# Kernel tuning notes

Hardware: AMD Instinct MI355X
Metric: run time of the kernel (lower is better)

Reference implementation:

```python
import jax, jax.numpy as jnp
import numpy as np

B = 2000           # number of events (segments)
N = 1_000_000      # total points (sum of num_points)
D_IN, H, D_OUT = 16, 256, 128
EPS = 1e-5


def _layer_norm(x, g, b):
    m = x.mean(-1, keepdims=True)
    v = x.var(-1, keepdims=True)
    return (x - m) * jax.lax.rsqrt(v + EPS) * g + b


def setup_inputs() -> dict:
    key = jax.random.key(0)
    ks = jax.random.split(key, 8)
    # ragged counts, all positive, summing exactly to N
    rng = np.random.default_rng(0)
    counts = np.full(B, N // B, dtype=np.int64)
    d = rng.integers(-400, 401, size=B // 2)
    counts[: B // 2] += d
    counts[B // 2 :] -= d
    assert counts.sum() == N and (counts > 0).all()
    z_t = jax.random.normal(ks[0], (N, D_IN), dtype=jnp.float32)
    def lin(k, fi, fo):
        return jax.random.normal(k, (fi, fo), dtype=jnp.float32) / np.sqrt(fi)
    return {
        "z_t": z_t,
        "W1": lin(ks[1], D_IN, H), "b1": jnp.zeros((H,), jnp.float32),
        "g1": jnp.ones((H,), jnp.float32), "be1": jnp.zeros((H,), jnp.float32),
        "W2": lin(ks[2], H, H), "b2": jnp.zeros((H,), jnp.float32),
        "g2": jnp.ones((H,), jnp.float32), "be2": jnp.zeros((H,), jnp.float32),
        "W3": lin(ks[3], H, D_OUT), "b3": jnp.zeros((D_OUT,), jnp.float32),
        "num_points": jnp.asarray(counts, dtype=jnp.int64),
    }


def reference(z_t, W1, b1, g1, be1, W2, b2, g2, be2, W3, b3, num_points):
    # per-point phi MLP: Linear -> LN -> ReLU (x2) -> Linear
    h = jax.nn.relu(_layer_norm(z_t @ W1 + b1, g1, be1))
    h = jax.nn.relu(_layer_norm(h @ W2 + b2, g2, be2))
    phi = h @ W3 + b3                                  # [N, D_OUT]
    # fused ragged mean-pool + broadcast back (replaces split/stack/repeat_interleave)
    seg = jnp.repeat(jnp.arange(B), num_points, total_repeat_length=N)  # [N]
    sums = jax.ops.segment_sum(phi, seg, num_segments=B)                # [B, D_OUT]
    emb = sums / num_points[:, None].astype(phi.dtype)                  # mean pooling
    return emb[seg]                                                     # [N, D_OUT]
```

## Files before the change

kernel.cpp:

```cpp
#include <hip/hip_runtime.h>
#include <hip/hip_bf16.h>
#include <cstdint>
#include <cstddef>

#define NPTS  1000000
#define BSEG  2000
#define DIN   16
#define HDIM  256
#define DOUT  128
#define NTILE (NPTS / 32)
#define NWG   512

typedef __bf16          bf16x8 __attribute__((ext_vector_type(8)));
typedef unsigned short  us16x8 __attribute__((ext_vector_type(8)));
typedef unsigned int    u32x4  __attribute__((ext_vector_type(4)));
typedef float           f32x4  __attribute__((ext_vector_type(4)));

static __device__ __forceinline__ unsigned short f2bf(float x) {
    unsigned int u = __float_as_uint(x);
    u += 0x7fffu + ((u >> 16) & 1u);
    return (unsigned short)(u >> 16);
}

static __device__ __forceinline__ bf16x8 ldb8(const unsigned short* p) {
    u32x4 v = *(const u32x4*)p;
    return __builtin_bit_cast(bf16x8, v);
}
static __device__ __forceinline__ f32x4 mfma16(bf16x8 a, bf16x8 b, f32x4 c) {
    return __builtin_amdgcn_mfma_f32_16x16x32_bf16(a, b, c, 0, 0, 0);
}
static __device__ __forceinline__ void keep(bf16x8& v) {
    u32x4 u = __builtin_bit_cast(u32x4, v);
    unsigned a0 = u[0], a1 = u[1], a2 = u[2], a3 = u[3];
    asm volatile("" : "+v"(a0), "+v"(a1), "+v"(a2), "+v"(a3));
    u32x4 r; r[0] = a0; r[1] = a1; r[2] = a2; r[3] = a3;
    v = __builtin_bit_cast(bf16x8, r);
}

static __device__ __forceinline__ float rsum16(float x) {
    x += __builtin_bit_cast(float, __builtin_amdgcn_update_dpp(
             0, __builtin_bit_cast(int, x), 0x128, 0xf, 0xf, false));
    x += __builtin_bit_cast(float, __builtin_amdgcn_update_dpp(
             0, __builtin_bit_cast(int, x), 0x124, 0xf, 0xf, false));
    x += __builtin_bit_cast(float, __builtin_amdgcn_update_dpp(
             0, __builtin_bit_cast(int, x), 0x122, 0xf, 0xf, false));
    x += __builtin_bit_cast(float, __builtin_amdgcn_update_dpp(
             0, __builtin_bit_cast(int, x), 0x121, 0xf, 0xf, false));
    return x;
}

__global__ __launch_bounds__(1024) void scan_counts(const int* __restrict__ counts,
                                                    int* __restrict__ offsets) {
    __shared__ int a[2048];
    const int t = threadIdx.x;
    a[t]        = (t        < BSEG) ? counts[t]        : 0;
    a[t + 1024] = (t + 1024 < BSEG) ? counts[t + 1024] : 0;
    for (int s = 1; s < 2048; s <<= 1) {
        __syncthreads();
        int x1 = (t >= s) ? a[t - s] : 0;
        int x2 = a[t + 1024 - s];
        __syncthreads();
        a[t] += x1;
        a[t + 1024] += x2;
    }
    __syncthreads();
    if (t == 0) offsets[0] = 0;
    offsets[t + 1] = a[t];
    if (t + 1024 < BSEG) offsets[t + 1025] = a[t + 1024];
}

__global__ __launch_bounds__(256) void fill_seg(const int* __restrict__ offsets,
                                                unsigned short* __restrict__ seg) {
    const int b  = blockIdx.x;
    const int lo = offsets[b], hi = offsets[b + 1];
    for (int i = lo + threadIdx.x; i < hi; i += 256) seg[i] = (unsigned short)b;
}

__global__ __launch_bounds__(256) void prep_weights(const float* __restrict__ W1,
                                                    const float* __restrict__ W2,
                                                    unsigned short* __restrict__ w1t,
                                                    unsigned short* __restrict__ w2t) {
    const int i = blockIdx.x * 256 + threadIdx.x;
    if (i < HDIM * 32) {
        int n = i >> 5, k = i & 31;
        w1t[i] = (k < DIN) ? f2bf(W1[k * HDIM + n]) : (unsigned short)0;
    } else {
        int j = i - HDIM * 32;
        if (j < HDIM * HDIM) {
            int n = j >> 8, k = j & 255;
            w2t[j] = f2bf(W2[k * HDIM + n]);
        }
    }
}

__global__ __launch_bounds__(256, 2) void fused_phi_pool(
    const float* __restrict__ z,
    const unsigned short* __restrict__ w1t,
    const unsigned short* __restrict__ w2t,
    const float* __restrict__ b1, const float* __restrict__ g1, const float* __restrict__ be1,
    const float* __restrict__ b2, const float* __restrict__ g2, const float* __restrict__ be2,
    const unsigned short* __restrict__ seg,
    float* __restrict__ sums_h) {
    __shared__ __align__(16) unsigned short h1[32][264];
    __shared__ __align__(16) float part[2][32][8];
    __shared__ __align__(16) int seg_sm[2][32];

    const int tid  = threadIdx.x;
    const int wave = tid >> 6;
    const int lane = tid & 63;
    const int l15  = lane & 15;
    const int quad = lane >> 4;
    const int colw = wave * 64 + l15;
    const bool zlane = (quad < 2);

    bf16x8 bw1[4];
    bf16x8 bw2[4][8];
#pragma unroll
    for (int t = 0; t < 4; ++t) {
        const int n = (wave * 4 + t) * 16 + l15;
        bw1[t] = ldb8(w1t + n * 32 + quad * 8);
        keep(bw1[t]);
#pragma unroll
        for (int ks = 0; ks < 8; ++ks) {
            bw2[t][ks] = ldb8(w2t + n * 256 + ks * 32 + quad * 8);
            keep(bw2[t][ks]);
        }
    }
    float b1v[4], g1v[4], e1v[4], b2v[4], g2v[4], e2v[4];
#pragma unroll
    for (int t = 0; t < 4; ++t) {
        const int c = colw + t * 16;
        b1v[t] = b1[c]; g1v[t] = g1[c]; e1v[t] = be1[c];
        b2v[t] = b2[c]; g2v[t] = g2[c]; e2v[t] = be2[c];
    }

    float4 zn[2][2];
    {
        const int base0 = blockIdx.x * 32;
        if (zlane) {
#pragma unroll
            for (int mb = 0; mb < 2; ++mb) {
                const float* zp = z + (size_t)(base0 + mb * 16 + l15) * DIN + quad * 8;
                zn[mb][0] = *(const float4*)zp;
                zn[mb][1] = *(const float4*)(zp + 4);
            }
        }
    }

    int p = 0;
    for (int tile = blockIdx.x; tile < NTILE; tile += NWG, p ^= 1) {
        const int base = tile * 32;
        if (tid < 32) seg_sm[p][tid] = (int)seg[base + tid];

        float4 zc[2][2];
#pragma unroll
        for (int mb = 0; mb < 2; ++mb) { zc[mb][0] = zn[mb][0]; zc[mb][1] = zn[mb][1]; }
        const int ntile = tile + NWG;
        if (zlane && ntile < NTILE) {
            const int nb = ntile * 32;
#pragma unroll
            for (int mb = 0; mb < 2; ++mb) {
                const float* zp = z + (size_t)(nb + mb * 16 + l15) * DIN + quad * 8;
                zn[mb][0] = *(const float4*)zp;
                zn[mb][1] = *(const float4*)(zp + 4);
            }
        }

        f32x4 a1[2][4];
#pragma unroll
        for (int mb = 0; mb < 2; ++mb) {
            bf16x8 af;
            if (zlane) {
                us16x8 u;
                u[0] = f2bf(zc[mb][0].x); u[1] = f2bf(zc[mb][0].y);
                u[2] = f2bf(zc[mb][0].z); u[3] = f2bf(zc[mb][0].w);
                u[4] = f2bf(zc[mb][1].x); u[5] = f2bf(zc[mb][1].y);
                u[6] = f2bf(zc[mb][1].z); u[7] = f2bf(zc[mb][1].w);
                af = __builtin_bit_cast(bf16x8, u);
            } else {
                us16x8 u = {0, 0, 0, 0, 0, 0, 0, 0};
                af = __builtin_bit_cast(bf16x8, u);
            }
            const f32x4 zero = {0.f, 0.f, 0.f, 0.f};
#pragma unroll
            for (int t = 0; t < 4; ++t) a1[mb][t] = mfma16(af, bw1[t], zero);
        }
#pragma unroll
        for (int mb = 0; mb < 2; ++mb) {
            float s[4], q[4];
#pragma unroll
            for (int r = 0; r < 4; ++r) {
                float sv = 0.f, qv = 0.f;
#pragma unroll
                for (int t = 0; t < 4; ++t) {
                    float y = a1[mb][t][r] + b1v[t];
                    a1[mb][t][r] = y;
                    sv += y; qv += y * y;
                }
                s[r] = rsum16(sv); q[r] = rsum16(qv);
            }
            if (l15 == 0) {
#pragma unroll
                for (int r = 0; r < 4; ++r)
                    *(float2*)&part[p][mb * 16 + quad * 4 + r][wave * 2] =
                        make_float2(s[r], q[r]);
            }
        }
        __syncthreads();
#pragma unroll
        for (int mb = 0; mb < 2; ++mb) {
#pragma unroll
            for (int r = 0; r < 4; ++r) {
                const int row = mb * 16 + quad * 4 + r;
                float4 pa = *(const float4*)&part[p][row][0];
                float4 pb = *(const float4*)&part[p][row][4];
                float st = pa.x + pa.z + pb.x + pb.z;
                float qt = pa.y + pa.w + pb.y + pb.w;
                float mean = st * (1.f / 256.f);
                float var  = qt * (1.f / 256.f) - mean * mean;
                float rs   = rsqrtf(fmaxf(var, 0.f) + 1e-5f);
#pragma unroll
                for (int t = 0; t < 4; ++t) {
                    float A = rs * g1v[t];
                    float y = fmaxf(fmaf(a1[mb][t][r], A, fmaf(-mean, A, e1v[t])), 0.f);
                    h1[row][colw + t * 16] = f2bf(y);
                }
            }
        }
        __syncthreads();

        f32x4 a2[2][4];
#pragma unroll
        for (int mb = 0; mb < 2; ++mb) {
            const f32x4 zero = {0.f, 0.f, 0.f, 0.f};
#pragma unroll
            for (int t = 0; t < 4; ++t) a2[mb][t] = zero;
#pragma unroll
            for (int ks = 0; ks < 8; ++ks) {
                bf16x8 af = ldb8(&h1[mb * 16 + l15][ks * 32 + quad * 8]);
#pragma unroll
                for (int t = 0; t < 4; ++t) a2[mb][t] = mfma16(af, bw2[t][ks], a2[mb][t]);
            }
        }
#pragma unroll
        for (int mb = 0; mb < 2; ++mb) {
            float s[4], q[4];
#pragma unroll
            for (int r = 0; r < 4; ++r) {
                float sv = 0.f, qv = 0.f;
#pragma unroll
                for (int t = 0; t < 4; ++t) {
                    float y = a2[mb][t][r] + b2v[t];
                    a2[mb][t][r] = y;
                    sv += y; qv += y * y;
                }
                s[r] = rsum16(sv); q[r] = rsum16(qv);
            }
            if (l15 == 0) {
#pragma unroll
                for (int r = 0; r < 4; ++r)
                    *(float2*)&part[p][mb * 16 + quad * 4 + r][wave * 2] =
                        make_float2(s[r], q[r]);
            }
        }
        __syncthreads();
#pragma unroll
        for (int mb = 0; mb < 2; ++mb) {
#pragma unroll
            for (int r = 0; r < 4; ++r) {
                const int row = mb * 16 + quad * 4 + r;
                float4 pa = *(const float4*)&part[p][row][0];
                float4 pb = *(const float4*)&part[p][row][4];
                float st = pa.x + pa.z + pb.x + pb.z;
                float qt = pa.y + pa.w + pb.y + pb.w;
                float mean = st * (1.f / 256.f);
                float var  = qt * (1.f / 256.f) - mean * mean;
                float rs   = rsqrtf(fmaxf(var, 0.f) + 1e-5f);
#pragma unroll
                for (int t = 0; t < 4; ++t) {
                    float A = rs * g2v[t];
                    a2[mb][t][r] =
                        fmaxf(fmaf(a2[mb][t][r], A, fmaf(-mean, A, e2v[t])), 0.f);
                }
            }
        }

        const int s0  = seg_sm[p][0];
        const int s31 = seg_sm[p][31];
        if (s0 == s31) {
#pragma unroll
            for (int t = 0; t < 4; ++t) {
                float cs = a2[0][t][0] + a2[0][t][1] + a2[0][t][2] + a2[0][t][3]
                         + a2[1][t][0] + a2[1][t][1] + a2[1][t][2] + a2[1][t][3];
                cs += __shfl_xor(cs, 16, 64);
                cs += __shfl_xor(cs, 32, 64);
                if (quad == 0)
                    atomicAdd(&sums_h[s0 * HDIM + colw + t * 16], cs);
            }
        } else {
            const int* sgp = &seg_sm[p][0];
            float m0[4], m1[4];
#pragma unroll
            for (int r = 0; r < 4; ++r) {
                m0[r] = (sgp[quad * 4 + r]      == s0) ? 1.f : 0.f;
                m1[r] = (sgp[16 + quad * 4 + r] == s0) ? 1.f : 0.f;
            }
#pragma unroll
            for (int t = 0; t < 4; ++t) {
                float cs = 0.f, ca = 0.f;
#pragma unroll
                for (int r = 0; r < 4; ++r) {
                    cs += a2[0][t][r] + a2[1][t][r];
                    ca = fmaf(a2[0][t][r], m0[r], ca);
                    ca = fmaf(a2[1][t][r], m1[r], ca);
                }
                cs += __shfl_xor(cs, 16, 64);
                cs += __shfl_xor(cs, 32, 64);
                ca += __shfl_xor(ca, 16, 64);
                ca += __shfl_xor(ca, 32, 64);
                if (quad == 0) {
                    atomicAdd(&sums_h[s0  * HDIM + colw + t * 16], ca);
                    atomicAdd(&sums_h[s31 * HDIM + colw + t * 16], cs - ca);
                }
            }
        }
    }
}

__global__ __launch_bounds__(256) void emb_gemm(const float* __restrict__ sums_h,
                                                const float* __restrict__ W3,
                                                const float* __restrict__ b3,
                                                const int* __restrict__ counts,
                                                float* __restrict__ emb) {
    const int b = blockIdx.x * 2 + (threadIdx.x >> 7);
    const int o = threadIdx.x & 127;
    const float* sh = sums_h + b * HDIM;
    float acc = 0.f;
#pragma unroll 8
    for (int k = 0; k < HDIM; ++k) acc = fmaf(sh[k], W3[k * DOUT + o], acc);
    emb[b * DOUT + o] = acc / (float)counts[b] + b3[o];
}

__global__ __launch_bounds__(256) void broadcast_out(const float* __restrict__ emb,
                                                     const unsigned short* __restrict__ seg,
                                                     float* __restrict__ out) {
    const int idx = blockIdx.x * 256 + threadIdx.x;
    const int n = idx >> 4, oct = idx & 15;
    const int s = seg[n];
    float4 v0 = ((const float4*)emb)[s * 32 + oct * 2];
    float4 v1 = ((const float4*)emb)[s * 32 + oct * 2 + 1];
    ((float4*)out)[idx * 2]     = v0;
    ((float4*)out)[idx * 2 + 1] = v1;
}

extern "C" void kernel_launch(void* const* d_in, const int* in_sizes, int n_in,
                              void* d_out, int out_size, void* d_ws, size_t ws_size,
                              hipStream_t stream) {
    const float* z   = (const float*)d_in[0];
    const float* W1  = (const float*)d_in[1];
    const float* b1  = (const float*)d_in[2];
    const float* g1  = (const float*)d_in[3];
    const float* be1 = (const float*)d_in[4];
    const float* W2  = (const float*)d_in[5];
    const float* b2  = (const float*)d_in[6];
    const float* g2  = (const float*)d_in[7];
    const float* be2 = (const float*)d_in[8];
    const float* W3  = (const float*)d_in[9];
    const float* b3  = (const float*)d_in[10];
    const int* counts = (const int*)d_in[11];
    float* out = (float*)d_out;

    char* ws = (char*)d_ws;
    float*          sums_h  = (float*)(ws);
    float*          emb     = (float*)(ws + 2048000);
    int*            offsets = (int*)  (ws + 3072000);
    unsigned short* seg     = (unsigned short*)(ws + 3080016);
    unsigned short* w1t     = (unsigned short*)(ws + 5080016);
    unsigned short* w2t     = (unsigned short*)(ws + 5096400);

    hipMemsetAsync(sums_h, 0, (size_t)BSEG * HDIM * sizeof(float), stream);
    scan_counts<<<1, 1024, 0, stream>>>(counts, offsets);
    fill_seg<<<BSEG, 256, 0, stream>>>(offsets, seg);
    prep_weights<<<(HDIM * 32 + HDIM * HDIM) / 256, 256, 0, stream>>>(W1, W2, w1t, w2t);
    fused_phi_pool<<<NWG, 256, 0, stream>>>(z, w1t, w2t,
                                            b1, g1, be1, b2, g2, be2,
                                            seg, sums_h);
    emb_gemm<<<BSEG / 2, 256, 0, stream>>>(sums_h, W3, b3, counts, emb);
    broadcast_out<<<NPTS * 16 / 256, 256, 0, stream>>>(emb, seg, out);
}
```

Before: 1.033 ms.

## Fold b1 into W1 MFMA, pack LayerNorm math, stage W1 in LDS

Folds bias b1 into the first GEMM by adding a constant-one input column, so the per-element bias add disappears. W1 fragments now sit in shared memory instead of registers, freeing VGPRs. LayerNorm statistics and normalization use packed f32 instructions, bf16 conversion uses v_cvt_pk_bf16_f32, and h1 is written with paired ds_write_b16 stores. The broadcast kernel switches to one float4 per thread with nontemporal stores. The costs are extra LDS traffic to reload W1 fragments every tile, a slightly larger LDS footprint, and bf16 rounding of b1.

```diff
diff --git a/kernel.cpp b/kernel.cpp
--- a/kernel.cpp
+++ b/kernel.cpp
@@ -15,6 +15,7 @@
 typedef unsigned short  us16x8 __attribute__((ext_vector_type(8)));
 typedef unsigned int    u32x4  __attribute__((ext_vector_type(4)));
 typedef float           f32x4  __attribute__((ext_vector_type(4)));
+typedef float           f32x2  __attribute__((ext_vector_type(2)));
 
 static __device__ __forceinline__ unsigned short f2bf(float x) {
     unsigned int u = __float_as_uint(x);
@@ -36,6 +37,24 @@
     u32x4 r; r[0] = a0; r[1] = a1; r[2] = a2; r[3] = a3;
     v = __builtin_bit_cast(bf16x8, r);
 }
+
+static __device__ __forceinline__ f32x2 pkadd(f32x2 a, f32x2 b) {
+    f32x2 d; asm("v_pk_add_f32 %0, %1, %2" : "=v"(d) : "v"(a), "v"(b)); return d;
+}
+static __device__ __forceinline__ f32x2 pkmul(f32x2 a, f32x2 b) {
+    f32x2 d; asm("v_pk_mul_f32 %0, %1, %2" : "=v"(d) : "v"(a), "v"(b)); return d;
+}
+static __device__ __forceinline__ f32x2 pkfma(f32x2 a, f32x2 b, f32x2 c) {
+    f32x2 d; asm("v_pk_fma_f32 %0, %1, %2, %3" : "=v"(d) : "v"(a), "v"(b), "v"(c)); return d;
+}
+static __device__ __forceinline__ f32x2 relu2(f32x2 a) {
+    f32x2 d; d[0] = fmaxf(a[0], 0.f); d[1] = fmaxf(a[1], 0.f); return d;
+}
+static __device__ __forceinline__ unsigned cvtpk(float a, float b) {
+    unsigned d; asm("v_cvt_pk_bf16_f32 %0, %1, %2" : "=v"(d) : "v"(a), "v"(b)); return d;
+}
+static __device__ __forceinline__ f32x2 lohalf(f32x4 v) { return __builtin_shufflevector(v, v, 0, 1); }
+static __device__ __forceinline__ f32x2 hihalf(f32x4 v) { return __builtin_shufflevector(v, v, 2, 3); }
 
 static __device__ __forceinline__ float rsum16(float x) {
     x += __builtin_bit_cast(float, __builtin_amdgcn_update_dpp(
@@ -77,13 +96,15 @@
 }
 
 __global__ __launch_bounds__(256) void prep_weights(const float* __restrict__ W1,
+                                                    const float* __restrict__ b1,
                                                     const float* __restrict__ W2,
                                                     unsigned short* __restrict__ w1t,
                                                     unsigned short* __restrict__ w2t) {
     const int i = blockIdx.x * 256 + threadIdx.x;
     if (i < HDIM * 32) {
         int n = i >> 5, k = i & 31;
-        w1t[i] = (k < DIN) ? f2bf(W1[k * HDIM + n]) : (unsigned short)0;
+        float v = (k < DIN) ? W1[k * HDIM + n] : ((k == DIN) ? b1[n] : 0.f);
+        w1t[i] = f2bf(v);
     } else {
         int j = i - HDIM * 32;
         if (j < HDIM * HDIM) {
@@ -97,13 +118,14 @@
     const float* __restrict__ z,
     const unsigned short* __restrict__ w1t,
     const unsigned short* __restrict__ w2t,
-    const float* __restrict__ b1, const float* __restrict__ g1, const float* __restrict__ be1,
+    const float* __restrict__ g1, const float* __restrict__ be1,
     const float* __restrict__ b2, const float* __restrict__ g2, const float* __restrict__ be2,
     const unsigned short* __restrict__ seg,
     float* __restrict__ sums_h) {
     __shared__ __align__(16) unsigned short h1[32][264];
-    __shared__ __align__(16) float part[2][32][8];
-    __shared__ __align__(16) int seg_sm[2][32];
+    __shared__ __align__(16) unsigned short w1l[HDIM * 32];
+    __shared__ __align__(16) float part2[2][2][8][20];
+    __shared__ int seg_sm[2][32];
 
     const int tid  = threadIdx.x;
     const int wave = tid >> 6;
@@ -113,26 +135,35 @@
     const int colw = wave * 64 + l15;
     const bool zlane = (quad < 2);
 
-    bf16x8 bw1[4];
+    {
+        const u32x4* src = (const u32x4*)w1t;
+        u32x4* dst = (u32x4*)w1l;
+        for (int i = tid; i < HDIM * 32 / 8; i += 256) dst[i] = src[i];
+    }
+
     bf16x8 bw2[4][8];
 #pragma unroll
     for (int t = 0; t < 4; ++t) {
         const int n = (wave * 4 + t) * 16 + l15;
-        bw1[t] = ldb8(w1t + n * 32 + quad * 8);
-        keep(bw1[t]);
 #pragma unroll
         for (int ks = 0; ks < 8; ++ks) {
             bw2[t][ks] = ldb8(w2t + n * 256 + ks * 32 + quad * 8);
             keep(bw2[t][ks]);
         }
     }
-    float b1v[4], g1v[4], e1v[4], b2v[4], g2v[4], e2v[4];
+
+    f32x2 gd1[4], ed1[4], gd2[4], ed2[4], bd2[4];
 #pragma unroll
     for (int t = 0; t < 4; ++t) {
         const int c = colw + t * 16;
-        b1v[t] = b1[c]; g1v[t] = g1[c]; e1v[t] = be1[c];
-        b2v[t] = b2[c]; g2v[t] = g2[c]; e2v[t] = be2[c];
-    }
+        float gv = g1[c];  gd1[t][0] = gv; gd1[t][1] = gv;
+        float ev = be1[c]; ed1[t][0] = ev; ed1[t][1] = ev;
+        float g2v = g2[c]; gd2[t][0] = g2v; gd2[t][1] = g2v;
+        float e2v = be2[c]; ed2[t][0] = e2v; ed2[t][1] = e2v;
+        float b2v = b2[c]; bd2[t][0] = b2v; bd2[t][1] = b2v;
+    }
+    const f32x2 zero2 = {0.f, 0.f};
+    const unsigned h1w = (unsigned)(size_t)&h1[quad * 4][colw];
 
     float4 zn[2][2];
     {
@@ -147,6 +178,8 @@
         }
     }
 
+    __syncthreads();
+
     int p = 0;
     for (int tile = blockIdx.x; tile < NTILE; tile += NWG, p ^= 1) {
         const int base = tile * 32;
@@ -166,67 +199,86 @@
             }
         }
 
+        bf16x8 w1f[4];
+#pragma unroll
+        for (int t = 0; t < 4; ++t)
+            w1f[t] = ldb8(&w1l[((wave * 4 + t) * 16 + l15) * 32 + quad * 8]);
+
         f32x4 a1[2][4];
 #pragma unroll
         for (int mb = 0; mb < 2; ++mb) {
             bf16x8 af;
             if (zlane) {
-                us16x8 u;
-                u[0] = f2bf(zc[mb][0].x); u[1] = f2bf(zc[mb][0].y);
-                u[2] = f2bf(zc[mb][0].z); u[3] = f2bf(zc[mb][0].w);
-                u[4] = f2bf(zc[mb][1].x); u[5] = f2bf(zc[mb][1].y);
-                u[6] = f2bf(zc[mb][1].z); u[7] = f2bf(zc[mb][1].w);
+                u32x4 u;
+                u[0] = cvtpk(zc[mb][0].x, zc[mb][0].y);
+                u[1] = cvtpk(zc[mb][0].z, zc[mb][0].w);
+                u[2] = cvtpk(zc[mb][1].x, zc[mb][1].y);
+                u[3] = cvtpk(zc[mb][1].z, zc[mb][1].w);
                 af = __builtin_bit_cast(bf16x8, u);
             } else {
-                us16x8 u = {0, 0, 0, 0, 0, 0, 0, 0};
+                u32x4 u = {(quad == 2) ? 0x3F80u : 0u, 0u, 0u, 0u};
                 af = __builtin_bit_cast(bf16x8, u);
             }
             const f32x4 zero = {0.f, 0.f, 0.f, 0.f};
 #pragma unroll
-            for (int t = 0; t < 4; ++t) a1[mb][t] = mfma16(af, bw1[t], zero);
-        }
-#pragma unroll
-        for (int mb = 0; mb < 2; ++mb) {
-            float s[4], q[4];
-#pragma unroll
-            for (int r = 0; r < 4; ++r) {
-                float sv = 0.f, qv = 0.f;
+            for (int t = 0; t < 4; ++t) a1[mb][t] = mfma16(af, w1f[t], zero);
+        }
+
+#pragma unroll
+        for (int mb = 0; mb < 2; ++mb)
+#pragma unroll
+            for (int rp = 0; rp < 2; ++rp) {
+                f32x2 sv = zero2, qv = zero2;
 #pragma unroll
                 for (int t = 0; t < 4; ++t) {
-                    float y = a1[mb][t][r] + b1v[t];
-                    a1[mb][t][r] = y;
-                    sv += y; qv += y * y;
-                }
-                s[r] = rsum16(sv); q[r] = rsum16(qv);
-            }
-            if (l15 == 0) {
-#pragma unroll
-                for (int r = 0; r < 4; ++r)
-                    *(float2*)&part[p][mb * 16 + quad * 4 + r][wave * 2] =
-                        make_float2(s[r], q[r]);
-            }
-        }
+                    f32x2 y = rp ? hihalf(a1[mb][t]) : lohalf(a1[mb][t]);
+                    sv = pkadd(sv, y);
+                    qv = pkfma(y, y, qv);
+                }
+                float sa = rsum16(sv[0]), sb = rsum16(sv[1]);
+                float qa = rsum16(qv[0]), qb = rsum16(qv[1]);
+                if (l15 == 0) {
+                    f32x2 s2 = {sa, sb};
+                    f32x2 q2 = {qa, qb};
+                    *(f32x2*)&part2[p][mb][quad * 2 + rp][wave * 2]     = s2;
+                    *(f32x2*)&part2[p][mb][quad * 2 + rp][8 + wave * 2] = q2;
+                }
+            }
         __syncthreads();
-#pragma unroll
-        for (int mb = 0; mb < 2; ++mb) {
-#pragma unroll
-            for (int r = 0; r < 4; ++r) {
-                const int row = mb * 16 + quad * 4 + r;
-                float4 pa = *(const float4*)&part[p][row][0];
-                float4 pb = *(const float4*)&part[p][row][4];
-                float st = pa.x + pa.z + pb.x + pb.z;
-                float qt = pa.y + pa.w + pb.y + pb.w;
-                float mean = st * (1.f / 256.f);
-                float var  = qt * (1.f / 256.f) - mean * mean;
-                float rs   = rsqrtf(fmaxf(var, 0.f) + 1e-5f);
+
+#pragma unroll
+        for (int mb = 0; mb < 2; ++mb)
+#pragma unroll
+            for (int rp = 0; rp < 2; ++rp) {
+                const float* pr = &part2[p][mb][quad * 2 + rp][0];
+                f32x4 sa4 = *(const f32x4*)pr;
+                f32x4 sb4 = *(const f32x4*)(pr + 4);
+                f32x4 qa4 = *(const f32x4*)(pr + 8);
+                f32x4 qb4 = *(const f32x4*)(pr + 12);
+                f32x2 st2 = pkadd(pkadd(lohalf(sa4), hihalf(sa4)),
+                                  pkadd(lohalf(sb4), hihalf(sb4)));
+                f32x2 qt2 = pkadd(pkadd(lohalf(qa4), hihalf(qa4)),
+                                  pkadd(lohalf(qb4), hihalf(qb4)));
+                float m0 = st2[0] * (1.f / 256.f), m1 = st2[1] * (1.f / 256.f);
+                float v0 = fmaf(qt2[0], 1.f / 256.f, -(m0 * m0));
+                float v1 = fmaf(qt2[1], 1.f / 256.f, -(m1 * m1));
+                float r0 = rsqrtf(fmaxf(v0, 0.f) + 1e-5f);
+                float r1 = rsqrtf(fmaxf(v1, 0.f) + 1e-5f);
+                f32x2 rs2 = {r0, r1};
+                f32x2 mn2 = {-m0, -m1};
 #pragma unroll
                 for (int t = 0; t < 4; ++t) {
-                    float A = rs * g1v[t];
-                    float y = fmaxf(fmaf(a1[mb][t][r], A, fmaf(-mean, A, e1v[t])), 0.f);
-                    h1[row][colw + t * 16] = f2bf(y);
-                }
-            }
-        }
+                    f32x2 A2 = pkmul(rs2, gd1[t]);
+                    f32x2 C2 = pkfma(mn2, A2, ed1[t]);
+                    f32x2 y  = rp ? hihalf(a1[mb][t]) : lohalf(a1[mb][t]);
+                    f32x2 h2 = relu2(pkfma(y, A2, C2));
+                    unsigned pkv  = cvtpk(h2[0], h2[1]);
+                    unsigned addr = h1w + (unsigned)(mb * 8448 + rp * 1056 + t * 32);
+                    asm volatile("ds_write_b16 %0, %1\n\t"
+                                 "ds_write_b16_d16_hi %0, %1 offset:528"
+                                 :: "v"(addr), "v"(pkv));
+                }
+            }
         __syncthreads();
 
         f32x4 a2[2][4];
@@ -243,47 +295,57 @@
             }
         }
 #pragma unroll
-        for (int mb = 0; mb < 2; ++mb) {
-            float s[4], q[4];
-#pragma unroll
-            for (int r = 0; r < 4; ++r) {
-                float sv = 0.f, qv = 0.f;
+        for (int mb = 0; mb < 2; ++mb)
+#pragma unroll
+            for (int rp = 0; rp < 2; ++rp) {
+                f32x2 sv = zero2, qv = zero2;
 #pragma unroll
                 for (int t = 0; t < 4; ++t) {
-                    float y = a2[mb][t][r] + b2v[t];
-                    a2[mb][t][r] = y;
-                    sv += y; qv += y * y;
-                }
-                s[r] = rsum16(sv); q[r] = rsum16(qv);
-            }
-            if (l15 == 0) {
-#pragma unroll
-                for (int r = 0; r < 4; ++r)
-                    *(float2*)&part[p][mb * 16 + quad * 4 + r][wave * 2] =
-                        make_float2(s[r], q[r]);
-            }
-        }
+                    f32x2 y = pkadd(rp ? hihalf(a2[mb][t]) : lohalf(a2[mb][t]), bd2[t]);
+                    sv = pkadd(sv, y);
+                    qv = pkfma(y, y, qv);
+                }
+                float sa = rsum16(sv[0]), sb = rsum16(sv[1]);
+                float qa = rsum16(qv[0]), qb = rsum16(qv[1]);
+                if (l15 == 0) {
+                    f32x2 s2 = {sa, sb};
+                    f32x2 q2 = {qa, qb};
+                    *(f32x2*)&part2[p][mb][quad * 2 + rp][wave * 2]     = s2;
+                    *(f32x2*)&part2[p][mb][quad * 2 + rp][8 + wave * 2] = q2;
+                }
+            }
         __syncthreads();
-#pragma unroll
-        for (int mb = 0; mb < 2; ++mb) {
-#pragma unroll
-            for (int r = 0; r < 4; ++r) {
-                const int row = mb * 16 + quad * 4 + r;
-                float4 pa = *(const float4*)&part[p][row][0];
-                float4 pb = *(const float4*)&part[p][row][4];
-                float st = pa.x + pa.z + pb.x + pb.z;
-                float qt = pa.y + pa.w + pb.y + pb.w;
-                float mean = st * (1.f / 256.f);
-                float var  = qt * (1.f / 256.f) - mean * mean;
-                float rs   = rsqrtf(fmaxf(var, 0.f) + 1e-5f);
+
+#pragma unroll
+        for (int mb = 0; mb < 2; ++mb)
+#pragma unroll
+            for (int rp = 0; rp < 2; ++rp) {
+                const float* pr = &part2[p][mb][quad * 2 + rp][0];
+                f32x4 sa4 = *(const f32x4*)pr;
+                f32x4 sb4 = *(const f32x4*)(pr + 4);
+                f32x4 qa4 = *(const f32x4*)(pr + 8);
+                f32x4 qb4 = *(const f32x4*)(pr + 12);
+                f32x2 st2 = pkadd(pkadd(lohalf(sa4), hihalf(sa4)),
+                                  pkadd(lohalf(sb4), hihalf(sb4)));
+                f32x2 qt2 = pkadd(pkadd(lohalf(qa4), hihalf(qa4)),
+                                  pkadd(lohalf(qb4), hihalf(qb4)));
+                float m0 = st2[0] * (1.f / 256.f), m1 = st2[1] * (1.f / 256.f);
+                float v0 = fmaf(qt2[0], 1.f / 256.f, -(m0 * m0));
+                float v1 = fmaf(qt2[1], 1.f / 256.f, -(m1 * m1));
+                float r0 = rsqrtf(fmaxf(v0, 0.f) + 1e-5f);
+                float r1 = rsqrtf(fmaxf(v1, 0.f) + 1e-5f);
+                f32x2 rs2 = {r0, r1};
+                f32x2 mn2 = {-m0, -m1};
 #pragma unroll
                 for (int t = 0; t < 4; ++t) {
-                    float A = rs * g2v[t];
-                    a2[mb][t][r] =
-                        fmaxf(fmaf(a2[mb][t][r], A, fmaf(-mean, A, e2v[t])), 0.f);
-                }
-            }
-        }
+                    f32x2 A2 = pkmul(rs2, gd2[t]);
+                    f32x2 C2 = pkfma(mn2, A2, ed2[t]);
+                    f32x2 y  = pkadd(rp ? hihalf(a2[mb][t]) : lohalf(a2[mb][t]), bd2[t]);
+                    f32x2 h2 = relu2(pkfma(y, A2, C2));
+                    a2[mb][t][rp * 2]     = h2[0];
+                    a2[mb][t][rp * 2 + 1] = h2[1];
+                }
+            }
 
         const int s0  = seg_sm[p][0];
         const int s31 = seg_sm[p][31];
@@ -299,11 +361,11 @@
             }
         } else {
             const int* sgp = &seg_sm[p][0];
-            float m0[4], m1[4];
+            float m0v[4], m1v[4];
 #pragma unroll
             for (int r = 0; r < 4; ++r) {
-                m0[r] = (sgp[quad * 4 + r]      == s0) ? 1.f : 0.f;
-                m1[r] = (sgp[16 + quad * 4 + r] == s0) ? 1.f : 0.f;
+                m0v[r] = (sgp[quad * 4 + r]      == s0) ? 1.f : 0.f;
+                m1v[r] = (sgp[16 + quad * 4 + r] == s0) ? 1.f : 0.f;
             }
 #pragma unroll
             for (int t = 0; t < 4; ++t) {
@@ -311,8 +373,8 @@
 #pragma unroll
                 for (int r = 0; r < 4; ++r) {
                     cs += a2[0][t][r] + a2[1][t][r];
-                    ca = fmaf(a2[0][t][r], m0[r], ca);
-                    ca = fmaf(a2[1][t][r], m1[r], ca);
+                    ca = fmaf(a2[0][t][r], m0v[r], ca);
+                    ca = fmaf(a2[1][t][r], m1v[r], ca);
                 }
                 cs += __shfl_xor(cs, 16, 64);
                 cs += __shfl_xor(cs, 32, 64);
@@ -345,12 +407,10 @@
                                                      const unsigned short* __restrict__ seg,
                                                      float* __restrict__ out) {
     const int idx = blockIdx.x * 256 + threadIdx.x;
-    const int n = idx >> 4, oct = idx & 15;
+    const int n = idx >> 5, c = idx & 31;
     const int s = seg[n];
-    float4 v0 = ((const float4*)emb)[s * 32 + oct * 2];
-    float4 v1 = ((const float4*)emb)[s * 32 + oct * 2 + 1];
-    ((float4*)out)[idx * 2]     = v0;
-    ((float4*)out)[idx * 2 + 1] = v1;
+    f32x4 v = ((const f32x4*)emb)[s * 32 + c];
+    __builtin_nontemporal_store(v, (f32x4*)out + idx);
 }
 
 extern "C" void kernel_launch(void* const* d_in, const int* in_sizes, int n_in,
@@ -381,10 +441,10 @@
     hipMemsetAsync(sums_h, 0, (size_t)BSEG * HDIM * sizeof(float), stream);
     scan_counts<<<1, 1024, 0, stream>>>(counts, offsets);
     fill_seg<<<BSEG, 256, 0, stream>>>(offsets, seg);
-    prep_weights<<<(HDIM * 32 + HDIM * HDIM) / 256, 256, 0, stream>>>(W1, W2, w1t, w2t);
+    prep_weights<<<(HDIM * 32 + HDIM * HDIM) / 256, 256, 0, stream>>>(W1, b1, W2, w1t, w2t);
     fused_phi_pool<<<NWG, 256, 0, stream>>>(z, w1t, w2t,
-                                            b1, g1, be1, b2, g2, be2,
+                                            g1, be1, b2, g2, be2,
                                             seg, sums_h);
     emb_gemm<<<BSEG / 2, 256, 0, stream>>>(sums_h, W3, b3, counts, emb);
-    broadcast_out<<<NPTS * 16 / 256, 256, 0, stream>>>(emb, seg, out);
-}
+    broadcast_out<<<NPTS * DOUT / 4 / 256, 256, 0, stream>>>(emb, seg, out);
+}
```

New measurement: 937.6 us. 1.1x faster.
